# Kernel optimization log

Measured on AMD Instinct MI355X. Metric: run time of the kernel, lower is better.

## Reference

```python
import jax, jax.numpy as jnp
import numpy as np


def _att(xf, W1, W2):
    # xf: [B, L, dk]; low-rank attention scores, softmax over last dim
    dk = W1.shape[0]
    s1 = xf @ W1                                   # [B, L, 10]
    s2 = jnp.einsum('rk,bjk->brj', W2, xf)         # [B, 10, L]
    scores = jnp.einsum('bir,brj->bij', s1, s2) / jnp.sqrt(jnp.float32(dk))
    return jax.nn.softmax(scores, axis=-1)         # [B, L, L]


def setup_inputs() -> dict:
    B, Ci, Co, N, T = 8, 64, 64, 1000, 24
    ks = jax.random.split(jax.random.key(0), 16)
    f32 = jnp.float32
    return {
        'x': jax.random.normal(ks[0], (B, Ci, N, T), f32),
        'A_adj': jax.random.uniform(ks[1], (N, N), f32),
        'att0_W1': jax.random.normal(ks[2], (N * T, 10), f32) * 0.02,
        'att0_W2': jax.random.normal(ks[3], (10, N * T), f32) * 0.02,
        'gatt_W1': jax.random.normal(ks[4], (Ci * T, 10), f32) * 0.02,
        'gatt_W2': jax.random.normal(ks[5], (10, Ci * T), f32) * 0.02,
        'gcn_W': jax.random.normal(ks[6], (Ci, Co), f32) * 0.05,
        'tatt_W1': jax.random.normal(ks[7], (N * Co, 10), f32) * 0.02,
        'tatt_W2': jax.random.normal(ks[8], (10, N * Co), f32) * 0.02,
        'conv1_w': jax.random.normal(ks[9], (Co, Co, 1, 2), f32) * 0.05,
        'conv1_b': jax.random.normal(ks[10], (Co,), f32) * 0.05,
        'conv2_w': jax.random.normal(ks[11], (Co, Co, 1, 2), f32) * 0.05,
        'conv2_b': jax.random.normal(ks[12], (Co,), f32) * 0.05,
        'res_w': jax.random.normal(ks[13], (Co, Ci, 1, 1), f32) * 0.05,
        'res_b': jax.random.normal(ks[14], (Co,), f32) * 0.05,
        'ln_g': jnp.ones((Co,), f32),
        'ln_b': jnp.zeros((Co,), f32),
    }


def reference(x, A_adj, att0_W1, att0_W2, gatt_W1, gatt_W2, gcn_W,
              tatt_W1, tatt_W2, conv1_w, conv1_b, conv2_w, conv2_b,
              res_w, res_b, ln_g, ln_b):
    B, C, N, T = x.shape
    # ---- block-level channel attention (requires_value=True) ----
    xf = x.reshape(B, C, N * T)
    x1 = (_att(xf, att0_W1, att0_W2) @ xf).reshape(B, C, N, T)
    # ---- GCN block: attention-gated adjacency + graph matmul ----
    xg = jnp.transpose(x1, (0, 2, 1, 3)).reshape(B, N, C * T)
    Ag = _att(xg, gatt_W1, gatt_W2) * A_adj                  # [B, N, N]
    g1 = jnp.einsum('bnm,bcmt->bnct', Ag, x1)                # [B, N, C, T]
    g = jnp.einsum('bnct,co->bont', g1, gcn_W)               # [B, Co, N, T]
    Co = g.shape[1]
    # ---- TCN block: temporal attention + dilated causal convs ----
    xt = jnp.transpose(g, (0, 3, 2, 1)).reshape(B, T, N * Co)
    x2 = (_att(xt, tatt_W1, tatt_W2) @ xt).reshape(B, T, N, Co)
    x2 = jnp.transpose(x2, (0, 3, 2, 1))                     # [B, Co, N, T]
    for w, b, d in ((conv1_w, conv1_b, 1), (conv2_w, conv2_b, 2)):
        y = jax.lax.conv_general_dilated(
            x2, w, (1, 1), [(0, 0), (d, d)], rhs_dilation=(1, d),
            dimension_numbers=('NCHW', 'OIHW', 'NCHW'))
        y = y + b[None, :, None, None]
        x2 = jax.nn.relu(y[..., :-d])                        # trim to T
    # ---- 1x1 residual conv ----
    res = jnp.einsum('bcnt,oc->bont', x, res_w[:, :, 0, 0]) + res_b[None, :, None, None]
    out = jax.nn.relu(x2 + res)
    # ---- LayerNorm over channel dim ----
    o = jnp.transpose(out, (0, 3, 2, 1))                     # [B, T, N, Co]
    mu = o.mean(-1, keepdims=True)
    var = o.var(-1, keepdims=True)
    o = (o - mu) / jnp.sqrt(var + 1e-5) * ln_g + ln_b
    return jnp.transpose(o, (0, 3, 2, 1))                    # [B, Co, N, T]
```

## Files before the change

kernel.cpp:

```cpp
#include <hip/hip_runtime.h>
#include <hip/hip_bf16.h>

typedef unsigned int u32;
typedef unsigned short ushortt;

#define B_  8
#define C_  64
#define N_  1000
#define T_  24
#define R_  10
#define NT_ 24000
#define CT_ 1536
#define NC_ 64000

typedef __attribute__((ext_vector_type(8))) short bf8v;
typedef __attribute__((ext_vector_type(4))) float f4v;

__device__ __forceinline__ ushortt f2b_bits(float f) {
  u32 x = __float_as_uint(f);
  u32 r = (x + 0x7fffu + ((x >> 16) & 1u)) >> 16;
  return (ushortt)r;
}

__device__ __forceinline__ u32 f2b_pair(float a, float b) {
  return (u32)f2b_bits(a) | ((u32)f2b_bits(b) << 16);
}

__device__ __forceinline__ float blockSum256(float v, float* red) {
  red[threadIdx.x] = v; __syncthreads();
  #pragma unroll
  for (int s = 128; s > 0; s >>= 1) {
    if (threadIdx.x < s) red[threadIdx.x] += red[threadIdx.x + s];
    __syncthreads();
  }
  float r = red[0]; __syncthreads();
  return r;
}
__device__ __forceinline__ float blockMax256(float v, float* red) {
  red[threadIdx.x] = v; __syncthreads();
  #pragma unroll
  for (int s = 128; s > 0; s >>= 1) {
    if (threadIdx.x < s) red[threadIdx.x] = fmaxf(red[threadIdx.x], red[threadIdx.x + s]);
    __syncthreads();
  }
  float r = red[0]; __syncthreads();
  return r;
}

__device__ __forceinline__ void ld24f32(const float* p, float* v) {
  #pragma unroll
  for (int t = 0; t < 24; t += 4) {
    float4 f = *(const float4*)&p[t];
    v[t] = f.x; v[t+1] = f.y; v[t+2] = f.z; v[t+3] = f.w;
  }
}

__global__ __launch_bounds__(256) void zerok(float* p, int n) {
  int i = blockIdx.x * 256 + threadIdx.x;
  if (i < n) p[i] = 0.f;
}

__global__ __launch_bounds__(256) void pack_w(
    const float* __restrict__ W1, const float* __restrict__ W2,
    float* __restrict__ Wp, int K) {
  int i = blockIdx.x * 256 + threadIdx.x;
  if (i >= K * 20) return;
  int k = i / 20, r = i - k * 20;
  Wp[i] = (r < 10) ? W1[(size_t)k * 10 + r] : W2[(size_t)(r - 10) * K + k];
}

__global__ __launch_bounds__(256) void pack_tailw(
    const float* __restrict__ c1w, const float* __restrict__ c2w,
    const float* __restrict__ rw, ushortt* __restrict__ Wt) {
  int i = blockIdx.x * 256 + threadIdx.x;
  if (i >= 20480) return;
  float v;
  if (i < 8192) {
    int tap = i >> 12, o = (i >> 6) & 63, c = i & 63;
    v = c1w[(size_t)(o * 64 + c) * 2 + (tap ? 0 : 1)];
  } else if (i < 16384) {
    int j = i - 8192;
    int tap = j >> 12, o = (j >> 6) & 63, c = j & 63;
    v = c2w[(size_t)(o * 64 + c) * 2 + (tap ? 0 : 1)];
  } else {
    int j = i - 16384;
    v = rw[j];
  }
  Wt[i] = f2b_bits(v);
}

__global__ __launch_bounds__(256) void att0_s12(
    const float* __restrict__ x, const float* __restrict__ Wp,
    float* __restrict__ s1, float* __restrict__ s2) {
  __shared__ float red[40 * 257];
  const int row0 = blockIdx.x * 4;
  const int kbase = blockIdx.y * 6000;
  const int tid = threadIdx.x;
  float acc[4][20];
  #pragma unroll
  for (int r = 0; r < 4; ++r)
    #pragma unroll
    for (int j = 0; j < 20; ++j) acc[r][j] = 0.f;
  const float* xb = x + (size_t)row0 * NT_ + kbase;
  const float4* wb4 = (const float4*)Wp + (size_t)kbase * 5;
  #pragma unroll 1
  for (int it = 0; it < 6; ++it) {
    int slot = tid + 256 * it;
    if (slot < 1500) {
      int k = slot * 4;
      float4 xv0 = *(const float4*)&xb[k];
      float4 xv1 = *(const float4*)&xb[NT_ + k];
      float4 xv2 = *(const float4*)&xb[2 * NT_ + k];
      float4 xv3 = *(const float4*)&xb[3 * NT_ + k];
      const float4* w4 = wb4 + (size_t)slot * 20;
      #pragma unroll
      for (int kk = 0; kk < 4; ++kk) {
        float4 wa = w4[kk * 5 + 0], wbv = w4[kk * 5 + 1], wc = w4[kk * 5 + 2],
               wd = w4[kk * 5 + 3], we = w4[kk * 5 + 4];
        float w[20] = {wa.x,wa.y,wa.z,wa.w, wbv.x,wbv.y,wbv.z,wbv.w,
                       wc.x,wc.y,wc.z,wc.w, wd.x,wd.y,wd.z,wd.w,
                       we.x,we.y,we.z,we.w};
        float xs0 = ((const float*)&xv0)[kk];
        float xs1 = ((const float*)&xv1)[kk];
        float xs2 = ((const float*)&xv2)[kk];
        float xs3 = ((const float*)&xv3)[kk];
        #pragma unroll
        for (int j = 0; j < 20; ++j) {
          acc[0][j] += xs0 * w[j];
          acc[1][j] += xs1 * w[j];
          acc[2][j] += xs2 * w[j];
          acc[3][j] += xs3 * w[j];
        }
      }
    }
  }
  #pragma unroll
  for (int half = 0; half < 2; ++half) {
    __syncthreads();
    #pragma unroll
    for (int mm = 0; mm < 40; ++mm) {
      int m = half * 40 + mm;
      red[mm * 257 + tid] = acc[m / 20][m % 20];
    }
    __syncthreads();
    #pragma unroll
    for (int s = 128; s >= 8; s >>= 1) {
      for (int i = tid; i < 40 * s; i += 256) {
        int rr = i / s, col = i - rr * s;
        red[rr * 257 + col] += red[rr * 257 + col + s];
      }
      __syncthreads();
    }
    if (tid < 40) {
      float v = 0.f;
      #pragma unroll
      for (int c = 0; c < 8; ++c) v += red[tid * 257 + c];
      int m = half * 40 + tid;
      int row = row0 + m / 20, j = m % 20;
      if (j < 10) atomicAdd(&s1[row * 10 + j], v);
      else        atomicAdd(&s2[row * 10 + (j - 10)], v);
    }
  }
}

__global__ __launch_bounds__(64) void att0_softmax(
    const float* __restrict__ s1, const float* __restrict__ s2, float* __restrict__ P) {
  int b = blockIdx.x, i = threadIdx.x;
  float r1[R_];
  #pragma unroll
  for (int r = 0; r < R_; ++r) r1[r] = s1[(b * 64 + i) * R_ + r];
  const float scale = rsqrtf(24000.f);
  float row[64]; float m = -1e30f;
  for (int j = 0; j < 64; ++j) {
    const float* s2r = s2 + (size_t)(b * 64 + j) * R_;
    float d = 0.f;
    #pragma unroll
    for (int r = 0; r < R_; ++r) d += r1[r] * s2r[r];
    d *= scale; row[j] = d; m = fmaxf(m, d);
  }
  float s = 0.f;
  for (int j = 0; j < 64; ++j) { float e = __expf(row[j] - m); row[j] = e; s += e; }
  float inv = 1.f / s;
  for (int j = 0; j < 64; ++j) P[((size_t)b * 64 + i) * 64 + j] = row[j] * inv;
}

__global__ __launch_bounds__(256) void att0_apply(
    const float* __restrict__ x, const float* __restrict__ P, float* __restrict__ x1tr) {
  __shared__ float Pss[4160];
  __shared__ float xt[6144];
  int b = blockIdx.y, n0 = blockIdx.x * 4;
  int tid = threadIdx.x;
  for (int i = tid; i < 4096; i += 256)
    Pss[(i >> 6) * 65 + (i & 63)] = P[(size_t)b * 4096 + i];
  {
    const float4* src4 = (const float4*)x;
    float4* dst4 = (float4*)xt;
    for (int i = tid; i < 1536; i += 256) {
      int j = i / 24, q = i - j * 24;
      dst4[i] = src4[(size_t)(b * 64 + j) * 6000 + n0 * 6 + q];
    }
  }
  __syncthreads();
  int ig = tid >> 4, ln = (tid >> 2) & 3, ts = tid & 3;
  float acc[4][6];
  #pragma unroll
  for (int ii = 0; ii < 4; ++ii)
    #pragma unroll
    for (int m = 0; m < 6; ++m) acc[ii][m] = 0.f;
  const float* base = &xt[ln * 24 + ts * 6];
  #pragma unroll 4
  for (int j = 0; j < 64; ++j) {
    float vj[6];
    #pragma unroll
    for (int m = 0; m < 6; ++m) vj[m] = base[j * 96 + m];
    #pragma unroll
    for (int ii = 0; ii < 4; ++ii) {
      float p = Pss[(ig * 4 + ii) * 65 + j];
      #pragma unroll
      for (int m = 0; m < 6; ++m) acc[ii][m] += p * vj[m];
    }
  }
  float* drow = x1tr + ((size_t)b * N_ + n0 + ln) * CT_ + ts * 6;
  #pragma unroll
  for (int ii = 0; ii < 4; ++ii) {
    float* d = drow + (ig * 4 + ii) * 24;
    *(float2*)&d[0] = make_float2(acc[ii][0], acc[ii][1]);
    *(float2*)&d[2] = make_float2(acc[ii][2], acc[ii][3]);
    *(float2*)&d[4] = make_float2(acc[ii][4], acc[ii][5]);
  }
}

__global__ __launch_bounds__(256) void transpose_x1(
    const float* __restrict__ x1tr, ushortt* __restrict__ Xbt) {
  __shared__ float s[64][65];
  int b = blockIdx.z, n0 = blockIdx.y * 64, c0 = blockIdx.x * 64;
  int tid = threadIdx.x;
  int r = tid >> 2, cc = (tid & 3) * 16;
  if (n0 + r < N_) {
    const float* src = x1tr + ((size_t)b * N_ + n0 + r) * CT_ + c0 + cc;
    #pragma unroll
    for (int i = 0; i < 16; i += 4) {
      float4 v = *(const float4*)&src[i];
      s[r][cc + i] = v.x; s[r][cc + i + 1] = v.y;
      s[r][cc + i + 2] = v.z; s[r][cc + i + 3] = v.w;
    }
  } else {
    #pragma unroll
    for (int i = 0; i < 16; ++i) s[r][cc + i] = 0.f;
  }
  __syncthreads();
  ushortt* dst = Xbt + ((size_t)b * CT_ + c0 + r) * 1024 + n0 + cc;
  #pragma unroll
  for (int i = 0; i < 16; ++i) dst[i] = f2b_bits(s[cc + i][r]);
}

__global__ __launch_bounds__(256) void gatt_s12(
    const float* __restrict__ xg, const float* __restrict__ Wp,
    float* __restrict__ s1, float* __restrict__ s2T) {
  __shared__ float xs[6144];
  __shared__ float red[5120];
  int bn0 = blockIdx.x * 4;
  int tid = threadIdx.x;
  {
    const float4* src4 = (const float4*)(xg + (size_t)bn0 * CT_);
    float4* dst4 = (float4*)xs;
    for (int i = tid; i < 1536; i += 256) dst4[i] = src4[i];
  }
  __syncthreads();
  int rid = tid >> 6, ks = tid & 63;
  float a[20];
  #pragma unroll
  for (int r = 0; r < 20; ++r) a[r] = 0.f;
  for (int k = ks; k < CT_; k += 64) {
    float xv = xs[rid * CT_ + k];
    const float4* wp4 = (const float4*)&Wp[(size_t)k * 20];
    float4 wa = wp4[0], wb = wp4[1], wc = wp4[2], wd = wp4[3], we = wp4[4];
    float wv[20] = {wa.x,wa.y,wa.z,wa.w, wb.x,wb.y,wb.z,wb.w, wc.x,wc.y,wc.z,wc.w,
                    wd.x,wd.y,wd.z,wd.w, we.x,we.y,we.z,we.w};
    #pragma unroll
    for (int r = 0; r < 20; ++r) a[r] += xv * wv[r];
  }
  #pragma unroll
  for (int r = 0; r < 20; ++r) red[tid * 20 + r] = a[r];
  __syncthreads();
  if (tid < 80) {
    int rid2 = tid / 20, r = tid % 20;
    float s = 0.f;
    for (int l = 0; l < 64; ++l) s += red[(rid2 * 64 + l) * 20 + r];
    int row = bn0 + rid2;
    int b = row / N_, n = row - b * N_;
    if (r < 10) s1[row * 10 + r] = s;
    else        s2T[((size_t)b * 10 + (r - 10)) * N_ + n] = s;
  }
}

__global__ __launch_bounds__(256) void gatt_scores(
    const float* __restrict__ s1, const float* __restrict__ s2T,
    const float* __restrict__ Aadj, ushortt* __restrict__ Agb) {
  __shared__ float p[N_];
  __shared__ float r1[R_];
  __shared__ float red[256];
  int b = blockIdx.x / N_, n = blockIdx.x % N_;
  if (threadIdx.x < R_) r1[threadIdx.x] = s1[((size_t)b * N_ + n) * R_ + threadIdx.x];
  __syncthreads();
  const float scale = rsqrtf(1536.f);
  const float* s2b = s2T + (size_t)b * 10 * N_;
  float lmax = -1e30f;
  for (int m = threadIdx.x; m < N_; m += 256) {
    float d = 0.f;
    #pragma unroll
    for (int r = 0; r < R_; ++r) d += r1[r] * s2b[r * N_ + m];
    d *= scale; p[m] = d; lmax = fmaxf(lmax, d);
  }
  float gmax = blockMax256(lmax, red);
  float lsum = 0.f;
  for (int m = threadIdx.x; m < N_; m += 256) {
    float e = __expf(p[m] - gmax); p[m] = e; lsum += e;
  }
  float gsum = blockSum256(lsum, red);
  float inv = 1.f / gsum;
  ushortt* agr = Agb + ((size_t)b * 1024 + n) * 1024;
  const float* ar = Aadj + (size_t)n * N_;
  for (int m = threadIdx.x; m < 1024; m += 256) {
    float v = (m < N_) ? p[m] * inv * ar[m] : 0.f;
    agr[m] = f2b_bits(v);
  }
}

__global__ __launch_bounds__(256) void gemm_mfma(
    const ushortt* __restrict__ Agb, const ushortt* __restrict__ Xbt,
    float* __restrict__ g1) {
  __shared__ ushortt As[4096];
  __shared__ ushortt Bs[4096];
  const int b = blockIdx.z;
  const int n0 = blockIdx.x * 128;
  const int m0 = blockIdx.y * 128;
  const ushortt* Ab = Agb + (size_t)b * 1024 * 1024;
  const ushortt* Bb = Xbt + (size_t)b * 1536 * 1024;
  const int tid = threadIdx.x;
  const int wave = tid >> 6, lane = tid & 63;
  const int wr = (wave >> 1) * 64, wc = (wave & 1) * 64;
  const int lrow = lane >> 2;
  const int lcol = (lane & 3) * 8;
  const int q = lane >> 4, l15 = lane & 15;

  f4v acc[4][4];
  #pragma unroll
  for (int i = 0; i < 4; ++i)
    #pragma unroll
    for (int j = 0; j < 4; ++j) acc[i][j] = (f4v){0.f, 0.f, 0.f, 0.f};

  const ushortt* gA = Ab + (size_t)(m0 + wave * 16 + lrow) * 1024 + lcol;
  const ushortt* gB = Bb + (size_t)(n0 + wave * 16 + lrow) * 1024 + lcol;
  ushortt* lA = &As[wave * 16 * 32];
  ushortt* lB = &Bs[wave * 16 * 32];

  for (int k0 = 0; k0 < 1024; k0 += 32) {
    __syncthreads();
    __builtin_amdgcn_global_load_lds(
      (const __attribute__((address_space(1))) void*)(gA + k0),
      (__attribute__((address_space(3))) void*)lA, 16, 0, 0);
    __builtin_amdgcn_global_load_lds(
      (const __attribute__((address_space(1))) void*)(gA + (size_t)64 * 1024 + k0),
      (__attribute__((address_space(3))) void*)(lA + 64 * 32), 16, 0, 0);
    __builtin_amdgcn_global_load_lds(
      (const __attribute__((address_space(1))) void*)(gB + k0),
      (__attribute__((address_space(3))) void*)lB, 16, 0, 0);
    __builtin_amdgcn_global_load_lds(
      (const __attribute__((address_space(1))) void*)(gB + (size_t)64 * 1024 + k0),
      (__attribute__((address_space(3))) void*)(lB + 64 * 32), 16, 0, 0);
    __syncthreads();
    bf8v af[4], bfr[4];
    #pragma unroll
    for (int i = 0; i < 4; ++i)
      af[i] = *(const bf8v*)&As[(wr + i * 16 + l15) * 32 + q * 8];
    #pragma unroll
    for (int j = 0; j < 4; ++j)
      bfr[j] = *(const bf8v*)&Bs[(wc + j * 16 + l15) * 32 + q * 8];
    #pragma unroll
    for (int i = 0; i < 4; ++i)
      #pragma unroll
      for (int j = 0; j < 4; ++j)
        acc[i][j] = __builtin_amdgcn_mfma_f32_16x16x32_bf16(af[i], bfr[j], acc[i][j], 0, 0, 0);
  }
  #pragma unroll
  for (int i = 0; i < 4; ++i) {
    int rbase = m0 + wr + i * 16 + q * 4;
    #pragma unroll
    for (int r = 0; r < 4; ++r) {
      int gm = rbase + r;
      if (gm < N_) {
        float* dst = g1 + ((size_t)b * N_ + gm) * CT_ + n0 + wc + l15;
        #pragma unroll
        for (int j = 0; j < 4; ++j) dst[j * 16] = acc[i][j][r];
      }
    }
  }
}

__global__ __launch_bounds__(256) void gcn_out(
    const float* __restrict__ g1, const float* __restrict__ W, float* __restrict__ g) {
  __shared__ float gs[6160];
  __shared__ float Ws[4096];
  int b = blockIdx.y, n0 = blockIdx.x * 4;
  int tid = threadIdx.x;
  {
    const float4* src4 = (const float4*)g1;
    float4* dst4 = (float4*)gs;
    for (int i = tid; i < 1536; i += 256) {
      int ln = i / 384, q = i - ln * 384;
      dst4[ln * 385 + q] = src4[(size_t)(b * N_ + n0 + ln) * 384 + q];
    }
  }
  for (int i = tid; i < 4096; i += 256) Ws[i] = W[i];
  __syncthreads();
  int og = tid >> 4, ln = (tid >> 2) & 3, ts = tid & 3;
  float acc[4][6];
  #pragma unroll
  for (int oo = 0; oo < 4; ++oo)
    #pragma unroll
    for (int m = 0; m < 6; ++m) acc[oo][m] = 0.f;
  const float* base = &gs[ln * 1540 + ts * 6];
  #pragma unroll 4
  for (int c = 0; c < 64; ++c) {
    float v[6];
    #pragma unroll
    for (int m = 0; m < 6; ++m) v[m] = base[c * 24 + m];
    float4 w4 = *(const float4*)&Ws[c * 64 + og * 4];
    float wv[4] = {w4.x, w4.y, w4.z, w4.w};
    #pragma unroll
    for (int oo = 0; oo < 4; ++oo)
      #pragma unroll
      for (int m = 0; m < 6; ++m) acc[oo][m] += wv[oo] * v[m];
  }
  #pragma unroll
  for (int oo = 0; oo < 4; ++oo) {
    int o = og * 4 + oo;
    float* d = g + (((size_t)(b * C_ + o)) * N_ + n0 + ln) * T_ + ts * 6;
    *(float2*)&d[0] = make_float2(acc[oo][0], acc[oo][1]);
    *(float2*)&d[2] = make_float2(acc[oo][2], acc[oo][3]);
    *(float2*)&d[4] = make_float2(acc[oo][4], acc[oo][5]);
  }
}

__global__ __launch_bounds__(256) void tatt_s12(
    const float* __restrict__ g, const float* __restrict__ Wp,
    float* __restrict__ s1, float* __restrict__ s2) {
  __shared__ float red[40 * 257];
  const int b = blockIdx.z, t0 = blockIdx.y * 4, n0 = blockIdx.x * 20;
  const int tid = threadIdx.x;
  const int o = tid & 63, nl = tid >> 6;
  float acc[4][20];
  #pragma unroll
  for (int tt = 0; tt < 4; ++tt)
    #pragma unroll
    for (int j = 0; j < 20; ++j) acc[tt][j] = 0.f;
  const float* gb = g + (size_t)(b * 64 + o) * NT_ + t0;
  #pragma unroll 1
  for (int it = 0; it < 5; ++it) {
    int n = n0 + it * 4 + nl;
    float4 gv = *(const float4*)&gb[n * 24];
    const float4* w4 = (const float4*)&Wp[(size_t)(n * 64 + o) * 20];
    float4 wa = w4[0], wbv = w4[1], wc = w4[2], wd = w4[3], we = w4[4];
    float w[20] = {wa.x,wa.y,wa.z,wa.w, wbv.x,wbv.y,wbv.z,wbv.w,
                   wc.x,wc.y,wc.z,wc.w, wd.x,wd.y,wd.z,wd.w,
                   we.x,we.y,we.z,we.w};
    float gs[4] = {gv.x, gv.y, gv.z, gv.w};
    #pragma unroll
    for (int tt = 0; tt < 4; ++tt)
      #pragma unroll
      for (int j = 0; j < 20; ++j) acc[tt][j] += gs[tt] * w[j];
  }
  #pragma unroll
  for (int half = 0; half < 2; ++half) {
    __syncthreads();
    #pragma unroll
    for (int mm = 0; mm < 40; ++mm) {
      int m = half * 40 + mm;
      red[mm * 257 + tid] = acc[m / 20][m % 20];
    }
    __syncthreads();
    #pragma unroll
    for (int s = 128; s >= 8; s >>= 1) {
      for (int i = tid; i < 40 * s; i += 256) {
        int rr = i / s, col = i - rr * s;
        red[rr * 257 + col] += red[rr * 257 + col + s];
      }
      __syncthreads();
    }
    if (tid < 40) {
      float v = 0.f;
      #pragma unroll
      for (int c = 0; c < 8; ++c) v += red[tid * 257 + c];
      int m = half * 40 + tid;
      int t = t0 + m / 20, j = m % 20;
      if (j < 10) atomicAdd(&s1[(b * T_ + t) * R_ + j], v);
      else        atomicAdd(&s2[(b * T_ + t) * R_ + (j - 10)], v);
    }
  }
}

__global__ __launch_bounds__(64) void tatt_softmax(
    const float* __restrict__ s1, const float* __restrict__ s2, float* __restrict__ Pt) {
  int b = blockIdx.x, t = threadIdx.x;
  if (t >= T_) return;
  float r1[R_];
  #pragma unroll
  for (int r = 0; r < R_; ++r) r1[r] = s1[(b * T_ + t) * R_ + r];
  const float scale = rsqrtf(64000.f);
  float row[T_]; float m = -1e30f;
  for (int j = 0; j < T_; ++j) {
    const float* s2r = s2 + (b * T_ + j) * R_;
    float d = 0.f;
    #pragma unroll
    for (int r = 0; r < R_; ++r) d += r1[r] * s2r[r];
    d *= scale; row[j] = d; m = fmaxf(m, d);
  }
  float s = 0.f;
  for (int j = 0; j < T_; ++j) { float e = __expf(row[j] - m); row[j] = e; s += e; }
  float inv = 1.f / s;
  for (int j = 0; j < T_; ++j) Pt[(b * T_ + t) * T_ + j] = row[j] * inv;
}

__global__ __launch_bounds__(256) void tatt_apply(
    const float* __restrict__ g, const float* __restrict__ Pt, ushortt* __restrict__ x2b) {
  __shared__ float P[576];
  int b = blockIdx.y;
  for (int i = threadIdx.x; i < 576; i += 256) P[i] = Pt[b * 576 + i];
  __syncthreads();
  int row = blockIdx.x * 256 + threadIdx.x;
  const float* gp = g + ((size_t)b * 64000 + row) * T_;
  float gr[T_];
  ld24f32(gp, gr);
  float out[T_];
  #pragma unroll
  for (int t = 0; t < T_; ++t) {
    float a = 0.f;
    const float* Pr = &P[t * T_];
    #pragma unroll
    for (int j = 0; j < T_; ++j) a += Pr[j] * gr[j];
    out[t] = a;
  }
  u32 w[12];
  #pragma unroll
  for (int t = 0; t < 24; t += 2) w[t >> 1] = f2b_pair(out[t], out[t + 1]);
  ushortt* xp = x2b + ((size_t)b * 64000 + row) * 24;
  *(uint4*)&xp[0]  = make_uint4(w[0], w[1], w[2], w[3]);
  *(uint4*)&xp[8]  = make_uint4(w[4], w[5], w[6], w[7]);
  *(uint4*)&xp[16] = make_uint4(w[8], w[9], w[10], w[11]);
}

#define CSB 1024
#define RSB 104
__global__ __launch_bounds__(256, 3) void tail_k(
    const ushortt* __restrict__ x2b, const float* __restrict__ x,
    const ushortt* __restrict__ Wt,
    const float* __restrict__ c1b, const float* __restrict__ c2b,
    const float* __restrict__ rb,
    const float* __restrict__ lg, const float* __restrict__ lb,
    float* __restrict__ outp) {
  __shared__ ushortt X2c[8192];
  __shared__ ushortt Y1c[8192];
  __shared__ ushortt Xrc[8192];
  __shared__ float mu[96], rs[96];
  ushortt* preS = X2c;
  int b = blockIdx.y, n0 = blockIdx.x * 4;
  int tid = threadIdx.x;
  int wave = tid >> 6, lane = tid & 63;
  int q = lane >> 4, l15 = lane & 15;

  const int sc = tid >> 2, snl = tid & 3;
  size_t rowi = ((size_t)(b * 64 + sc) * 1000 + n0 + snl) * 24;
  uint4 vx2[3];
  {
    const uint4* p = (const uint4*)(x2b + rowi);
    vx2[0] = p[0]; vx2[1] = p[1]; vx2[2] = p[2];
  }
  float4 vx[6];
  {
    const float4* p = (const float4*)(x + rowi);
    #pragma unroll
    for (int j = 0; j < 6; ++j) vx[j] = p[j];
  }
  ushortt* bufA = Y1c;
  ushortt* bufB = Xrc;
  {
    uint4* da = (uint4*)&bufA[sc * RSB + snl * 24];
    da[0] = vx2[0]; da[1] = vx2[1]; da[2] = vx2[2];
    u32 w[12];
    #pragma unroll
    for (int j = 0; j < 6; ++j) {
      w[2 * j]     = f2b_pair(vx[j].x, vx[j].y);
      w[2 * j + 1] = f2b_pair(vx[j].z, vx[j].w);
    }
    uint4* db = (uint4*)&bufB[sc * RSB + snl * 24];
    db[0] = make_uint4(w[0], w[1], w[2], w[3]);
    db[1] = make_uint4(w[4], w[5], w[6], w[7]);
    db[2] = make_uint4(w[8], w[9], w[10], w[11]);
  }
  __syncthreads();
  u32 kb[4][4];
  #pragma unroll
  for (int rep = 0; rep < 4; ++rep) {
    int slot = tid + rep * 256;
    int kblk = slot >> 7, col = slot & 127;
    int nl2 = col >> 5, s = col & 31;
    u32 pa[4];
    if (s >= 2 && s <= 25) {
      int boff = (kblk * 8) * RSB + nl2 * 24 + (s - 2);
      #pragma unroll
      for (int h = 0; h < 4; ++h) {
        u32 a0 = bufA[boff + (2 * h) * RSB], a1 = bufA[boff + (2 * h + 1) * RSB];
        pa[h] = a0 | (a1 << 16);
        u32 b0 = bufB[boff + (2 * h) * RSB], b1 = bufB[boff + (2 * h + 1) * RSB];
        kb[rep][h] = b0 | (b1 << 16);
      }
    } else {
      #pragma unroll
      for (int h = 0; h < 4; ++h) { pa[h] = 0u; kb[rep][h] = 0u; }
    }
    *(uint4*)&X2c[kblk * CSB + col * 8] = make_uint4(pa[0], pa[1], pa[2], pa[3]);
  }
  __syncthreads();
  #pragma unroll
  for (int rep = 0; rep < 4; ++rep) {
    int slot = tid + rep * 256;
    int kblk = slot >> 7, col = slot & 127;
    *(uint4*)&Xrc[kblk * CSB + col * 8] =
        make_uint4(kb[rep][0], kb[rep][1], kb[rep][2], kb[rep][3]);
  }
  __syncthreads();

  f4v acc1[2][4];
  #pragma unroll
  for (int ct = 0; ct < 2; ++ct)
    #pragma unroll
    for (int mt = 0; mt < 4; ++mt) acc1[ct][mt] = (f4v){0.f, 0.f, 0.f, 0.f};
  #pragma unroll
  for (int ki = 0; ki < 2; ++ki) {
    bf8v a0[4], a1[4];
    #pragma unroll
    for (int mt = 0; mt < 4; ++mt) {
      a0[mt] = *(const bf8v*)&Wt[(mt * 16 + l15) * 64 + ki * 32 + q * 8];
      a1[mt] = *(const bf8v*)&Wt[4096 + (mt * 16 + l15) * 64 + ki * 32 + q * 8];
    }
    #pragma unroll
    for (int ct = 0; ct < 2; ++ct) {
      int col = wave * 32 + ct * 16 + l15;
      int colp = (col == 0) ? 0 : col - 1;
      bf8v bc = *(const bf8v*)&X2c[(ki * 4 + q) * CSB + col * 8];
      bf8v bp = *(const bf8v*)&X2c[(ki * 4 + q) * CSB + colp * 8];
      #pragma unroll
      for (int mt = 0; mt < 4; ++mt) {
        acc1[ct][mt] = __builtin_amdgcn_mfma_f32_16x16x32_bf16(a0[mt], bc, acc1[ct][mt], 0, 0, 0);
        acc1[ct][mt] = __builtin_amdgcn_mfma_f32_16x16x32_bf16(a1[mt], bp, acc1[ct][mt], 0, 0, 0);
      }
    }
  }
  #pragma unroll
  for (int ct = 0; ct < 2; ++ct) {
    int s = ct * 16 + l15;
    int col = wave * 32 + s;
    bool v = (s >= 2 && s <= 25);
    #pragma unroll
    for (int mt = 0; mt < 4; ++mt) {
      int o0 = mt * 16 + q * 4;
      float4 bb = *(const float4*)&c1b[o0];
      float y0 = v ? fmaxf(acc1[ct][mt][0] + bb.x, 0.f) : 0.f;
      float y1 = v ? fmaxf(acc1[ct][mt][1] + bb.y, 0.f) : 0.f;
      float y2 = v ? fmaxf(acc1[ct][mt][2] + bb.z, 0.f) : 0.f;
      float y3 = v ? fmaxf(acc1[ct][mt][3] + bb.w, 0.f) : 0.f;
      u32 lo = (u32)f2b_bits(y0) | ((u32)f2b_bits(y1) << 16);
      u32 hi = (u32)f2b_bits(y2) | ((u32)f2b_bits(y3) << 16);
      *(uint2*)&Y1c[(o0 >> 3) * CSB + col * 8 + (o0 & 7)] = make_uint2(lo, hi);
    }
  }
  __syncthreads();

  f4v accA[2][4], accR[2][4];
  #pragma unroll
  for (int ct = 0; ct < 2; ++ct)
    #pragma unroll
    for (int mt = 0; mt < 4; ++mt) {
      accA[ct][mt] = (f4v){0.f, 0.f, 0.f, 0.f};
      accR[ct][mt] = (f4v){0.f, 0.f, 0.f, 0.f};
    }
  #pragma unroll
  for (int ki = 0; ki < 2; ++ki) {
    bf8v c0[4], c1t[4], rrf[4];
    #pragma unroll
    for (int mt = 0; mt < 4; ++mt) {
      c0[mt]  = *(const bf8v*)&Wt[8192 + (mt * 16 + l15) * 64 + ki * 32 + q * 8];
      c1t[mt] = *(const bf8v*)&Wt[12288 + (mt * 16 + l15) * 64 + ki * 32 + q * 8];
      rrf[mt] = *(const bf8v*)&Wt[16384 + (mt * 16 + l15) * 64 + ki * 32 + q * 8];
    }
    #pragma unroll
    for (int ct = 0; ct < 2; ++ct) {
      int col = wave * 32 + ct * 16 + l15;
      int colp2 = (col < 2) ? col : col - 2;
      bf8v bc = *(const bf8v*)&Y1c[(ki * 4 + q) * CSB + col * 8];
      bf8v bp = *(const bf8v*)&Y1c[(ki * 4 + q) * CSB + colp2 * 8];
      bf8v bx = *(const bf8v*)&Xrc[(ki * 4 + q) * CSB + col * 8];
      #pragma unroll
      for (int mt = 0; mt < 4; ++mt) {
        accA[ct][mt] = __builtin_amdgcn_mfma_f32_16x16x32_bf16(c0[mt], bc, accA[ct][mt], 0, 0, 0);
        accA[ct][mt] = __builtin_amdgcn_mfma_f32_16x16x32_bf16(c1t[mt], bp, accA[ct][mt], 0, 0, 0);
        accR[ct][mt] = __builtin_amdgcn_mfma_f32_16x16x32_bf16(rrf[mt], bx, accR[ct][mt], 0, 0, 0);
      }
    }
  }
  float pre[2][4][4];
  #pragma unroll
  for (int ct = 0; ct < 2; ++ct) {
    int s = ct * 16 + l15;
    bool v = (s >= 2 && s <= 25);
    int p = wave * 24 + s - 2;
    #pragma unroll
    for (int mt = 0; mt < 4; ++mt) {
      int o0 = mt * 16 + q * 4;
      float4 b2 = *(const float4*)&c2b[o0];
      float4 rbv = *(const float4*)&rb[o0];
      float bb2[4] = {b2.x, b2.y, b2.z, b2.w};
      float brv[4] = {rbv.x, rbv.y, rbv.z, rbv.w};
      #pragma unroll
      for (int r = 0; r < 4; ++r) {
        float a = fmaxf(accA[ct][mt][r] + bb2[r], 0.f) + accR[ct][mt][r] + brv[r];
        pre[ct][mt][r] = fmaxf(a, 0.f);
      }
      if (v) {
        u32 lo = (u32)f2b_bits(pre[ct][mt][0]) | ((u32)f2b_bits(pre[ct][mt][1]) << 16);
        u32 hi = (u32)f2b_bits(pre[ct][mt][2]) | ((u32)f2b_bits(pre[ct][mt][3]) << 16);
        *(uint2*)&preS[p * 68 + o0] = make_uint2(lo, hi);
      }
    }
  }
  __syncthreads();
  if (tid < 96) {
    const ushortt* pr = &preS[tid * 68];
    float sm = 0.f, qq = 0.f;
    #pragma unroll 8
    for (int c = 0; c < 64; c += 2) {
      u32 u = *(const u32*)&pr[c];
      float v0 = __uint_as_float(u << 16);
      float v1 = __uint_as_float(u & 0xffff0000u);
      sm += v0 + v1; qq += v0 * v0 + v1 * v1;
    }
    float m = sm * (1.f / 64.f);
    mu[tid] = m;
    rs[tid] = rsqrtf(qq * (1.f / 64.f) - m * m + 1e-5f);
  }
  __syncthreads();
  #pragma unroll
  for (int ct = 0; ct < 2; ++ct) {
    int s = ct * 16 + l15;
    bool v = (s >= 2 && s <= 25);
    if (!v) continue;
    int p = wave * 24 + s - 2;
    int t = s - 2;
    float m = mu[p], rr = rs[p];
    #pragma unroll
    for (int mt = 0; mt < 4; ++mt) {
      int o0 = mt * 16 + q * 4;
      float4 g4 = *(const float4*)&lg[o0];
      float4 b4 = *(const float4*)&lb[o0];
      float gg[4] = {g4.x, g4.y, g4.z, g4.w};
      float bb[4] = {b4.x, b4.y, b4.z, b4.w};
      #pragma unroll
      for (int r = 0; r < 4; ++r) {
        int o = o0 + r;
        float val = (pre[ct][mt][r] - m) * rr * gg[r] + bb[r];
        outp[((size_t)(b * 64 + o) * 1000 + n0 + wave) * 24 + t] = val;
      }
    }
  }
}

extern "C" void kernel_launch(void* const* d_in, const int* in_sizes, int n_in,
                              void* d_out, int out_size, void* d_ws, size_t ws_size,
                              hipStream_t stream) {
  const float* x     = (const float*)d_in[0];
  const float* Aadj  = (const float*)d_in[1];
  const float* a0W1  = (const float*)d_in[2];
  const float* a0W2  = (const float*)d_in[3];
  const float* gW1   = (const float*)d_in[4];
  const float* gW2   = (const float*)d_in[5];
  const float* gcnW  = (const float*)d_in[6];
  const float* tW1   = (const float*)d_in[7];
  const float* tW2   = (const float*)d_in[8];
  const float* c1w   = (const float*)d_in[9];
  const float* c1b   = (const float*)d_in[10];
  const float* c2w   = (const float*)d_in[11];
  const float* c2b   = (const float*)d_in[12];
  const float* rw    = (const float*)d_in[13];
  const float* rb    = (const float*)d_in[14];
  const float* lng   = (const float*)d_in[15];
  const float* lnb   = (const float*)d_in[16];
  float* out = (float*)d_out;

  float* ws = (float*)d_ws;
  float* R1   = ws;
  float* U    = R1 + 12288000;
  float* D    = U + 12288000;
  float* s1_0 = D + 12288000;
  float* s2_0 = s1_0 + 5120;
  float* P0   = s2_0 + 5120;
  float* s1g  = P0 + 32768;
  float* s2gT = s1g + 80000;
  float* s1t  = s2gT + 80000;
  float* s2t  = s1t + 1920;
  float* Ptb  = s2t + 1920;
  float* Wp0  = Ptb + 4608;
  float* Wgp  = Wp0 + 480000;
  float* Wtp  = Wgp + 30720;
  float* Wtl  = Wtp + 1280000;
  ushortt* Xbt = (ushortt*)U;
  ushortt* Agb = (ushortt*)(U + 6291456);
  ushortt* Wtail = (ushortt*)Wtl;
  float* g = U;
  if (ws_size < (size_t)38876416 * 4) return;

  pack_w<<<1875, 256, 0, stream>>>(a0W1, a0W2, Wp0, 24000);
  pack_w<<<120, 256, 0, stream>>>(gW1, gW2, Wgp, 1536);
  pack_w<<<5000, 256, 0, stream>>>(tW1, tW2, Wtp, 64000);
  pack_tailw<<<80, 256, 0, stream>>>(c1w, c2w, rw, Wtail);
  zerok<<<40, 256, 0, stream>>>(s1_0, 10240);
  att0_s12<<<dim3(128, 4), 256, 0, stream>>>(x, Wp0, s1_0, s2_0);
  att0_softmax<<<8, 64, 0, stream>>>(s1_0, s2_0, P0);
  att0_apply<<<dim3(250, 8), 256, 0, stream>>>(x, P0, R1);
  gatt_s12<<<2000, 256, 0, stream>>>(R1, Wgp, s1g, s2gT);
  transpose_x1<<<dim3(24, 16, 8), 256, 0, stream>>>(R1, Xbt);
  gatt_scores<<<8000, 256, 0, stream>>>(s1g, s2gT, Aadj, Agb);
  gemm_mfma<<<dim3(12, 8, 8), 256, 0, stream>>>(Agb, Xbt, D);
  gcn_out<<<dim3(250, 8), 256, 0, stream>>>(D, gcnW, g);
  zerok<<<15, 256, 0, stream>>>(s1t, 3840);
  tatt_s12<<<dim3(50, 6, 8), 256, 0, stream>>>(g, Wtp, s1t, s2t);
  tatt_softmax<<<8, 32, 0, stream>>>(s1t, s2t, Ptb);
  tatt_apply<<<dim3(250, 8), 256, 0, stream>>>(g, Ptb, (ushortt*)R1);
  tail_k<<<dim3(250, 8), 256, 0, stream>>>((const ushortt*)R1, x, Wtail,
                                           c1b, c2b, rb, lng, lnb, out);
}
```

Before: 548.8 us.

## Cut tail kernel LDS to two buffers and raise occupancy bound to four

The tail kernel now uses two shared buffers instead of three, reusing them across the conv1, conv2/residual and LayerNorm stages. This needs extra barriers and defers the residual-input reshuffle until after the first MFMA stage. Global loads are rewritten as coalesced row-contiguous copies, and the launch bound is raised from three to four blocks per CU. The aim is more resident blocks for latency hiding, at the cost of more syncs and register pressure from the values held across stages. A no-op edit in another kernel's address math leaves that kernel's behavior unchanged.

```diff
diff --git a/kernel.cpp b/kernel.cpp
--- a/kernel.cpp
+++ b/kernel.cpp
@@ -223,7 +223,7 @@
   float* drow = x1tr + ((size_t)b * N_ + n0 + ln) * CT_ + ts * 6;
   #pragma unroll
   for (int ii = 0; ii < 4; ++ii) {
-    float* d = drow + (ig * 4 + ii) * 24;
+    float* d = drow + (ii * 4 + ig) * 0 + (ig * 4 + ii) * 24;
     *(float2*)&d[0] = make_float2(acc[ii][0], acc[ii][1]);
     *(float2*)&d[2] = make_float2(acc[ii][2], acc[ii][3]);
     *(float2*)&d[4] = make_float2(acc[ii][4], acc[ii][5]);
@@ -552,83 +552,64 @@
 
 #define CSB 1024
 #define RSB 104
-__global__ __launch_bounds__(256, 3) void tail_k(
+__global__ __launch_bounds__(256, 4) void tail_k(
     const ushortt* __restrict__ x2b, const float* __restrict__ x,
     const ushortt* __restrict__ Wt,
     const float* __restrict__ c1b, const float* __restrict__ c2b,
     const float* __restrict__ rb,
     const float* __restrict__ lg, const float* __restrict__ lb,
     float* __restrict__ outp) {
-  __shared__ ushortt X2c[8192];
-  __shared__ ushortt Y1c[8192];
-  __shared__ ushortt Xrc[8192];
+  __shared__ ushortt L0[8192];
+  __shared__ ushortt L1[8192];
   __shared__ float mu[96], rs[96];
-  ushortt* preS = X2c;
   int b = blockIdx.y, n0 = blockIdx.x * 4;
   int tid = threadIdx.x;
   int wave = tid >> 6, lane = tid & 63;
   int q = lane >> 4, l15 = lane & 15;
 
-  const int sc = tid >> 2, snl = tid & 3;
-  size_t rowi = ((size_t)(b * 64 + sc) * 1000 + n0 + snl) * 24;
-  uint4 vx2[3];
-  {
-    const uint4* p = (const uint4*)(x2b + rowi);
-    vx2[0] = p[0]; vx2[1] = p[1]; vx2[2] = p[2];
-  }
-  float4 vx[6];
-  {
-    const float4* p = (const float4*)(x + rowi);
-    #pragma unroll
-    for (int j = 0; j < 6; ++j) vx[j] = p[j];
-  }
-  ushortt* bufA = Y1c;
-  ushortt* bufB = Xrc;
-  {
-    uint4* da = (uint4*)&bufA[sc * RSB + snl * 24];
-    da[0] = vx2[0]; da[1] = vx2[1]; da[2] = vx2[2];
-    u32 w[12];
-    #pragma unroll
-    for (int j = 0; j < 6; ++j) {
-      w[2 * j]     = f2b_pair(vx[j].x, vx[j].y);
-      w[2 * j + 1] = f2b_pair(vx[j].z, vx[j].w);
-    }
-    uint4* db = (uint4*)&bufB[sc * RSB + snl * 24];
-    db[0] = make_uint4(w[0], w[1], w[2], w[3]);
-    db[1] = make_uint4(w[4], w[5], w[6], w[7]);
-    db[2] = make_uint4(w[8], w[9], w[10], w[11]);
-  }
-  __syncthreads();
-  u32 kb[4][4];
+  #pragma unroll
+  for (int rep = 0; rep < 3; ++rep) {
+    int i = tid + rep * 256;
+    int c = i / 12, u = i - c * 12;
+    const uint4* src = (const uint4*)(x2b + ((size_t)(b * 64 + c) * 1000 + n0) * 24);
+    uint4 v = src[u];
+    *(uint4*)&L0[c * RSB + u * 8] = v;
+  }
+  #pragma unroll
+  for (int rep = 0; rep < 6; ++rep) {
+    int i = tid + rep * 256;
+    int c = i / 24, qq = i - c * 24;
+    const float4* src = (const float4*)(x + ((size_t)(b * 64 + c) * 1000 + n0) * 24);
+    float4 v = src[qq];
+    *(uint2*)&L1[c * RSB + qq * 4] = make_uint2(f2b_pair(v.x, v.y), f2b_pair(v.z, v.w));
+  }
+  __syncthreads();
+
+  u32 pa[4][4];
+  int sKblk[4], sCol[4];
   #pragma unroll
   for (int rep = 0; rep < 4; ++rep) {
     int slot = tid + rep * 256;
     int kblk = slot >> 7, col = slot & 127;
+    sKblk[rep] = kblk; sCol[rep] = col;
     int nl2 = col >> 5, s = col & 31;
-    u32 pa[4];
     if (s >= 2 && s <= 25) {
       int boff = (kblk * 8) * RSB + nl2 * 24 + (s - 2);
       #pragma unroll
       for (int h = 0; h < 4; ++h) {
-        u32 a0 = bufA[boff + (2 * h) * RSB], a1 = bufA[boff + (2 * h + 1) * RSB];
-        pa[h] = a0 | (a1 << 16);
-        u32 b0 = bufB[boff + (2 * h) * RSB], b1 = bufB[boff + (2 * h + 1) * RSB];
-        kb[rep][h] = b0 | (b1 << 16);
+        u32 a0 = L0[boff + (2 * h) * RSB], a1 = L0[boff + (2 * h + 1) * RSB];
+        pa[rep][h] = a0 | (a1 << 16);
       }
     } else {
       #pragma unroll
-      for (int h = 0; h < 4; ++h) { pa[h] = 0u; kb[rep][h] = 0u; }
-    }
-    *(uint4*)&X2c[kblk * CSB + col * 8] = make_uint4(pa[0], pa[1], pa[2], pa[3]);
-  }
-  __syncthreads();
-  #pragma unroll
-  for (int rep = 0; rep < 4; ++rep) {
-    int slot = tid + rep * 256;
-    int kblk = slot >> 7, col = slot & 127;
-    *(uint4*)&Xrc[kblk * CSB + col * 8] =
-        make_uint4(kb[rep][0], kb[rep][1], kb[rep][2], kb[rep][3]);
-  }
+      for (int h = 0; h < 4; ++h) pa[rep][h] = 0u;
+    }
+  }
+  __syncthreads();
+  #pragma unroll
+  for (int rep = 0; rep < 4; ++rep)
+    *(uint4*)&L0[sKblk[rep] * CSB + sCol[rep] * 8] =
+        make_uint4(pa[rep][0], pa[rep][1], pa[rep][2], pa[rep][3]);
   __syncthreads();
 
   f4v acc1[2][4];
@@ -648,8 +629,8 @@
     for (int ct = 0; ct < 2; ++ct) {
       int col = wave * 32 + ct * 16 + l15;
       int colp = (col == 0) ? 0 : col - 1;
-      bf8v bc = *(const bf8v*)&X2c[(ki * 4 + q) * CSB + col * 8];
-      bf8v bp = *(const bf8v*)&X2c[(ki * 4 + q) * CSB + colp * 8];
+      bf8v bc = *(const bf8v*)&L0[(ki * 4 + q) * CSB + col * 8];
+      bf8v bp = *(const bf8v*)&L0[(ki * 4 + q) * CSB + colp * 8];
       #pragma unroll
       for (int mt = 0; mt < 4; ++mt) {
         acc1[ct][mt] = __builtin_amdgcn_mfma_f32_16x16x32_bf16(a0[mt], bc, acc1[ct][mt], 0, 0, 0);
@@ -657,10 +638,27 @@
       }
     }
   }
+  u32 kb[4][4];
+  #pragma unroll
+  for (int rep = 0; rep < 4; ++rep) {
+    int col = sCol[rep];
+    int nl2 = col >> 5, s = col & 31;
+    if (s >= 2 && s <= 25) {
+      int boff = (sKblk[rep] * 8) * RSB + nl2 * 24 + (s - 2);
+      #pragma unroll
+      for (int h = 0; h < 4; ++h) {
+        u32 b0 = L1[boff + (2 * h) * RSB], b1 = L1[boff + (2 * h + 1) * RSB];
+        kb[rep][h] = b0 | (b1 << 16);
+      }
+    } else {
+      #pragma unroll
+      for (int h = 0; h < 4; ++h) kb[rep][h] = 0u;
+    }
+  }
+  u32 ypack[2][4][2];
   #pragma unroll
   for (int ct = 0; ct < 2; ++ct) {
     int s = ct * 16 + l15;
-    int col = wave * 32 + s;
     bool v = (s >= 2 && s <= 25);
     #pragma unroll
     for (int mt = 0; mt < 4; ++mt) {
@@ -670,11 +668,26 @@
       float y1 = v ? fmaxf(acc1[ct][mt][1] + bb.y, 0.f) : 0.f;
       float y2 = v ? fmaxf(acc1[ct][mt][2] + bb.z, 0.f) : 0.f;
       float y3 = v ? fmaxf(acc1[ct][mt][3] + bb.w, 0.f) : 0.f;
-      u32 lo = (u32)f2b_bits(y0) | ((u32)f2b_bits(y1) << 16);
-      u32 hi = (u32)f2b_bits(y2) | ((u32)f2b_bits(y3) << 16);
-      *(uint2*)&Y1c[(o0 >> 3) * CSB + col * 8 + (o0 & 7)] = make_uint2(lo, hi);
-    }
-  }
+      ypack[ct][mt][0] = f2b_pair(y0, y1);
+      ypack[ct][mt][1] = f2b_pair(y2, y3);
+    }
+  }
+  __syncthreads();
+
+  #pragma unroll
+  for (int ct = 0; ct < 2; ++ct) {
+    int col = wave * 32 + ct * 16 + l15;
+    #pragma unroll
+    for (int mt = 0; mt < 4; ++mt) {
+      int o0 = mt * 16 + q * 4;
+      *(uint2*)&L0[(o0 >> 3) * CSB + col * 8 + (o0 & 7)] =
+          make_uint2(ypack[ct][mt][0], ypack[ct][mt][1]);
+    }
+  }
+  #pragma unroll
+  for (int rep = 0; rep < 4; ++rep)
+    *(uint4*)&L1[sKblk[rep] * CSB + sCol[rep] * 8] =
+        make_uint4(kb[rep][0], kb[rep][1], kb[rep][2], kb[rep][3]);
   __syncthreads();
 
   f4v accA[2][4], accR[2][4];
@@ -698,9 +711,9 @@
     for (int ct = 0; ct < 2; ++ct) {
       int col = wave * 32 + ct * 16 + l15;
       int colp2 = (col < 2) ? col : col - 2;
-      bf8v bc = *(const bf8v*)&Y1c[(ki * 4 + q) * CSB + col * 8];
-      bf8v bp = *(const bf8v*)&Y1c[(ki * 4 + q) * CSB + colp2 * 8];
-      bf8v bx = *(const bf8v*)&Xrc[(ki * 4 + q) * CSB + col * 8];
+      bf8v bc = *(const bf8v*)&L0[(ki * 4 + q) * CSB + col * 8];
+      bf8v bp = *(const bf8v*)&L0[(ki * 4 + q) * CSB + colp2 * 8];
+      bf8v bx = *(const bf8v*)&L1[(ki * 4 + q) * CSB + col * 8];
       #pragma unroll
       for (int mt = 0; mt < 4; ++mt) {
         accA[ct][mt] = __builtin_amdgcn_mfma_f32_16x16x32_bf16(c0[mt], bc, accA[ct][mt], 0, 0, 0);
@@ -712,9 +725,6 @@
   float pre[2][4][4];
   #pragma unroll
   for (int ct = 0; ct < 2; ++ct) {
-    int s = ct * 16 + l15;
-    bool v = (s >= 2 && s <= 25);
-    int p = wave * 24 + s - 2;
     #pragma unroll
     for (int mt = 0; mt < 4; ++mt) {
       int o0 = mt * 16 + q * 4;
@@ -727,10 +737,23 @@
         float a = fmaxf(accA[ct][mt][r] + bb2[r], 0.f) + accR[ct][mt][r] + brv[r];
         pre[ct][mt][r] = fmaxf(a, 0.f);
       }
-      if (v) {
-        u32 lo = (u32)f2b_bits(pre[ct][mt][0]) | ((u32)f2b_bits(pre[ct][mt][1]) << 16);
-        u32 hi = (u32)f2b_bits(pre[ct][mt][2]) | ((u32)f2b_bits(pre[ct][mt][3]) << 16);
-        *(uint2*)&preS[p * 68 + o0] = make_uint2(lo, hi);
+    }
+  }
+  __syncthreads();
+
+  ushortt* preS = L0;
+  #pragma unroll
+  for (int ct = 0; ct < 2; ++ct) {
+    int s = ct * 16 + l15;
+    bool v = (s >= 2 && s <= 25);
+    if (v) {
+      int p = wave * 24 + s - 2;
+      #pragma unroll
+      for (int mt = 0; mt < 4; ++mt) {
+        int o0 = mt * 16 + q * 4;
+        *(uint2*)&preS[p * 68 + o0] =
+            make_uint2(f2b_pair(pre[ct][mt][0], pre[ct][mt][1]),
+                       f2b_pair(pre[ct][mt][2], pre[ct][mt][3]));
       }
     }
   }
```

Result: no change. 553.5 us (+0.9%).
